# Kernel optimization log

Measured on AMD Instinct MI355X. Metric: run time of the kernel, lower is better.

The kernel has to match this reference:

```python
import jax, jax.numpy as jnp
import numpy as np

EMBED = 64
HEADS = 8
N, S = 8, 1024


def setup_inputs() -> dict:
    key = jax.random.key(0)
    ks = jax.random.split(key, 8)
    scale = 1.0 / np.sqrt(EMBED)
    return {
        "values": jax.random.normal(ks[0], (N, S, EMBED), dtype=jnp.float32),
        "keys": jax.random.normal(ks[1], (N, S, EMBED), dtype=jnp.float32),
        "queries": jax.random.normal(ks[2], (N, S, EMBED), dtype=jnp.float32),
        # per-head projection weights, torch Linear convention: y = x @ W.T
        "Wv": jax.random.normal(ks[3], (HEADS, EMBED, EMBED), dtype=jnp.float32) * scale,
        "Wk": jax.random.normal(ks[4], (HEADS, EMBED, EMBED), dtype=jnp.float32) * scale,
        "Wq": jax.random.normal(ks[5], (HEADS, EMBED, EMBED), dtype=jnp.float32) * scale,
        "Wout": jax.random.normal(ks[6], (EMBED, HEADS * EMBED), dtype=jnp.float32) * (1.0 / np.sqrt(HEADS * EMBED)),
        "bout": jnp.zeros((EMBED,), dtype=jnp.float32),
    }


def reference(values, keys, queries, Wv, Wk, Wq, Wout, bout):
    d = queries.shape[-1]
    # Batched per-head projections (each head keeps full embed dim, per the module)
    v = jnp.einsum("nkd,hed->nhke", values, Wv)   # [N,H,K,D]
    k = jnp.einsum("nkd,hed->nhke", keys, Wk)     # [N,H,K,D]
    q = jnp.einsum("nqd,hed->nhqe", queries, Wq)  # [N,H,Q,D]
    energy = jnp.einsum("nhqd,nhkd->nhqk", q, k)
    attn = jax.nn.softmax(energy / jnp.sqrt(jnp.asarray(d, energy.dtype)), axis=-1)  # [N,H,Q,K]
    head_out = jnp.einsum("nhqk,nhkd->nhqd", attn, v)  # [N,H,Q,D]
    # torch.cat(output_heads, dim=2) == transpose heads next to feature then flatten
    nN, nH, nQ, nD = head_out.shape
    cat = jnp.transpose(head_out, (0, 2, 1, 3)).reshape(nN, nQ, nH * nD)  # [N,Q,H*D]
    out = cat @ Wout.T + bout  # [N,Q,D]
    return out, attn
```

## Files before the change

### kernel.cpp

```cpp
#include <hip/hip_runtime.h>

typedef __bf16 bf16x8 __attribute__((ext_vector_type(8)));
typedef __bf16 bf16x4 __attribute__((ext_vector_type(4)));
typedef float  f32x4  __attribute__((ext_vector_type(4)));

#define MFMA16(a, b, c) __builtin_amdgcn_mfma_f32_16x16x32_bf16((a), (b), (c), 0, 0, 0)

constexpr int N_ = 8, H_ = 8, S_ = 1024, D_ = 64;

__global__ __launch_bounds__(256) void proj_kernel(
    const float* __restrict__ Xq, const float* __restrict__ Xk,
    const float* __restrict__ Xv,
    const float* __restrict__ Wq, const float* __restrict__ Wk,
    const float* __restrict__ Wv,
    unsigned short* __restrict__ qb_, unsigned short* __restrict__ kb_,
    unsigned short* __restrict__ vtb_)
{
    __shared__ __bf16 T[64 * 72];

    const int which = blockIdx.y;
    const float* X = (which == 0) ? Xq : (which == 1) ? Xk : Xv;
    const float* W = (which == 0) ? Wq : (which == 1) ? Wk : Wv;

    const int b   = blockIdx.x;
    const int st  = b & 15;
    const int h   = (b >> 4) & 7;
    const int n   = b >> 7;
    const int s0  = st * 64;
    const int nh  = n * H_ + h;
    const int tid = threadIdx.x;
    const int w = tid >> 6, lane = tid & 63;
    const int l16 = lane & 15, quad = lane >> 4;

    const float* xrow = X + (size_t)(n * S_ + s0 + w * 16 + l16) * D_;
    bf16x8 a[2];
#pragma unroll
    for (int half = 0; half < 2; ++half) {
        const float* p = xrow + half * 32 + quad * 8;
        f32x4 x0 = *(const f32x4*)p;
        f32x4 x1 = *(const f32x4*)(p + 4);
#pragma unroll
        for (int j = 0; j < 4; ++j) { a[half][j] = (__bf16)x0[j]; a[half][4 + j] = (__bf16)x1[j]; }
    }

#pragma unroll
    for (int et = 0; et < 4; ++et) {
        const int e0 = et * 16;
        f32x4 acc = {0.f, 0.f, 0.f, 0.f};
#pragma unroll
        for (int half = 0; half < 2; ++half) {
            const float* wp = W + ((size_t)(h * 64 + e0 + l16)) * 64 + half * 32 + quad * 8;
            f32x4 x0 = *(const f32x4*)wp;
            f32x4 x1 = *(const f32x4*)(wp + 4);
            bf16x8 bf;
#pragma unroll
            for (int j = 0; j < 4; ++j) { bf[j] = (__bf16)x0[j]; bf[4 + j] = (__bf16)x1[j]; }
            acc = MFMA16(a[half], bf, acc);
        }
#pragma unroll
        for (int r = 0; r < 4; ++r) {
            const int sl = w * 16 + quad * 4 + r;
            const int e  = e0 + l16;
            const __bf16 v = (__bf16)acc[r];
            if (which == 2) T[e * 72 + sl] = v;
            else            T[sl * 72 + e] = v;
        }
    }
    __syncthreads();

    const int row = tid >> 2, seg = tid & 3;
    const bf16x8 d0 = *(const bf16x8*)&T[row * 72 + seg * 16];
    const bf16x8 d1 = *(const bf16x8*)&T[row * 72 + seg * 16 + 8];
    __bf16* dst;
    if (which == 2)
        dst = (__bf16*)vtb_ + ((size_t)nh * 64 + row) * S_ + s0 + seg * 16;
    else
        dst = (__bf16*)(which == 0 ? qb_ : kb_) + ((size_t)nh * S_ + s0 + row) * D_ + seg * 16;
    *(bf16x8*)dst = d0;
    *(bf16x8*)(dst + 8) = d1;
}

__global__ __launch_bounds__(256, 8) void attn_kernel(
    const unsigned short* __restrict__ qb_, const unsigned short* __restrict__ kb_,
    const unsigned short* __restrict__ vtb_,
    float* __restrict__ attn_out, unsigned short* __restrict__ catb_)
{
    __shared__ float Sred[4 * 16];
    __shared__ float Ored[2 * 16 * 68];

    const __bf16* qb  = (const __bf16*)qb_;
    const __bf16* kb  = (const __bf16*)kb_;
    const __bf16* vtb = (const __bf16*)vtb_;
    __bf16* catb = (__bf16*)catb_;

    const int bid = blockIdx.x;
    const int b   = (bid & 7) * 256 + (bid >> 3);
    const int qt  = b & 31;
    const int h   = (b >> 5) & 7;
    const int n   = b >> 8;
    const int nh  = n * H_ + h;
    const int q0  = qt * 32;

    const int tid = threadIdx.x;
    const int w = tid >> 6, lane = tid & 63;
    const int l16 = lane & 15, quad = lane >> 4;
    const int rw = w & 1;
    const int kw = w >> 1;
    const int k0 = kw * 512;

    const __bf16* qbase = qb + ((size_t)(nh * S_ + q0 + rw * 16 + l16)) * D_;
    const bf16x8 aq0 = *(const bf16x8*)(qbase + quad * 8);
    const bf16x8 aq1 = *(const bf16x8*)(qbase + 32 + quad * 8);

    const __bf16* kbase = kb + ((size_t)(nh * S_ + k0 + l16)) * D_ + quad * 8;

    float ssum = 0.f;
#pragma unroll 4
    for (int kt = 0; kt < 32; ++kt) {
        const __bf16* kp = kbase + (size_t)kt * 16 * D_;
        const bf16x8 b0 = *(const bf16x8*)kp;
        const bf16x8 b1 = *(const bf16x8*)(kp + 32);
        f32x4 c = {0.f, 0.f, 0.f, 0.f};
        c = MFMA16(b0, aq0, c);
        c = MFMA16(b1, aq1, c);
#pragma unroll
        for (int r = 0; r < 4; ++r) ssum += __expf(c[r] * 0.125f);
    }
    ssum += __shfl_xor(ssum, 16);
    ssum += __shfl_xor(ssum, 32);
    if (lane < 16) Sred[w * 16 + lane] = ssum;
    __syncthreads();
    const float inv = 1.0f / (Sred[w * 16 + l16] + Sred[(w ^ 2) * 16 + l16]);

    float* abase = attn_out + ((size_t)(nh * S_ + q0 + rw * 16 + l16)) * S_ + k0;
    const __bf16* vbase = vtb + ((size_t)(nh * 64 + l16)) * S_ + k0 + quad * 8;

    const int lo_addr = (((quad & 1) * 2) * 16 + l16) * 4;
    const int hi_addr = lo_addr + 64;
    const bool hiq = (quad & 2) != 0;

    f32x4 acc[4] = {{0.f,0.f,0.f,0.f},{0.f,0.f,0.f,0.f},{0.f,0.f,0.f,0.f},{0.f,0.f,0.f,0.f}};

#pragma unroll 2
    for (int ch = 0; ch < 16; ++ch) {
        unsigned Wt[2][2];
#pragma unroll
        for (int t = 0; t < 2; ++t) {
            const int kt = ch * 2 + t;
            const __bf16* kp = kbase + (size_t)kt * 16 * D_;
            const bf16x8 b0 = *(const bf16x8*)kp;
            const bf16x8 b1 = *(const bf16x8*)(kp + 32);
            f32x4 c = {0.f, 0.f, 0.f, 0.f};
            c = MFMA16(b0, aq0, c);
            c = MFMA16(b1, aq1, c);
            float p[4];
#pragma unroll
            for (int r = 0; r < 4; ++r) p[r] = __expf(c[r] * 0.125f) * inv;
#pragma unroll
            for (int pr = 0; pr < 2; ++pr) {
                const __bf16 ha = (__bf16)p[2 * pr], hb = (__bf16)p[2 * pr + 1];
                const unsigned ua = *(const unsigned short*)&ha;
                const unsigned ub = *(const unsigned short*)&hb;
                Wt[t][pr] = ua | (ub << 16);
            }
        }
        const int s00 = __builtin_amdgcn_ds_bpermute(lo_addr, (int)Wt[0][0]);
        const int s10 = __builtin_amdgcn_ds_bpermute(lo_addr, (int)Wt[1][0]);
        const int s01 = __builtin_amdgcn_ds_bpermute(lo_addr, (int)Wt[0][1]);
        const int s11 = __builtin_amdgcn_ds_bpermute(lo_addr, (int)Wt[1][1]);
        const int s02 = __builtin_amdgcn_ds_bpermute(hi_addr, (int)Wt[0][0]);
        const int s12 = __builtin_amdgcn_ds_bpermute(hi_addr, (int)Wt[1][0]);
        const int s03 = __builtin_amdgcn_ds_bpermute(hi_addr, (int)Wt[0][1]);
        const int s13 = __builtin_amdgcn_ds_bpermute(hi_addr, (int)Wt[1][1]);
        union { bf16x8 v; unsigned u[4]; } pf;
        pf.u[0] = (unsigned)(hiq ? s10 : s00);
        pf.u[1] = (unsigned)(hiq ? s11 : s01);
        pf.u[2] = (unsigned)(hiq ? s12 : s02);
        pf.u[3] = (unsigned)(hiq ? s13 : s03);

#pragma unroll
        for (int et = 0; et < 4; ++et) {
            const bf16x8 bv = *(const bf16x8*)(vbase + (size_t)et * 16 * S_ + ch * 32);
            acc[et] = MFMA16(pf.v, bv, acc[et]);
        }

        f32x4 f0, f1;
#pragma unroll
        for (int j = 0; j < 4; ++j) { f0[j] = (float)pf.v[j]; f1[j] = (float)pf.v[4 + j]; }
        float* ap = abase + ch * 32 + quad * 8;
        *(f32x4*)ap = f0;
        *(f32x4*)(ap + 4) = f1;
    }

    __syncthreads();
    if (kw == 1) {
#pragma unroll
        for (int et = 0; et < 4; ++et)
#pragma unroll
            for (int r = 0; r < 4; ++r)
                Ored[rw * (16 * 68) + (quad * 4 + r) * 68 + et * 16 + l16] = acc[et][r];
    }
    __syncthreads();
    if (kw == 0) {
#pragma unroll
        for (int r = 0; r < 4; ++r) {
            const int s = q0 + rw * 16 + quad * 4 + r;
            __bf16* cp = catb + ((size_t)n * S_ + s) * (H_ * D_) + h * D_ + l16;
#pragma unroll
            for (int et = 0; et < 4; ++et) {
                const float o = acc[et][r] +
                    Ored[rw * (16 * 68) + (quad * 4 + r) * 68 + et * 16 + l16];
                cp[et * 16] = (__bf16)o;
            }
        }
    }
}

__global__ __launch_bounds__(256) void outproj_kernel(
    const unsigned short* __restrict__ catb_, const float* __restrict__ Wout,
    const float* __restrict__ bout, float* __restrict__ out)
{
    __shared__ float R[4 * 16 * 68];

    const __bf16* catb = (const __bf16*)catb_;
    const int r0  = blockIdx.x * 16;
    const int tid = threadIdx.x;
    const int w = tid >> 6, lane = tid & 63;
    const int l16 = lane & 15, quad = lane >> 4;
    const int k0 = w * 128;

    const __bf16* arow  = catb + (size_t)(r0 + l16) * 512 + k0 + quad * 8;
    const float*  wbase = Wout + (size_t)l16 * 512 + k0 + quad * 8;

    f32x4 acc[4] = {{0.f,0.f,0.f,0.f},{0.f,0.f,0.f,0.f},{0.f,0.f,0.f,0.f},{0.f,0.f,0.f,0.f}};

#pragma unroll
    for (int kc = 0; kc < 4; ++kc) {
        const bf16x8 af = *(const bf16x8*)(arow + kc * 32);
#pragma unroll
        for (int et = 0; et < 4; ++et) {
            const float* wp = wbase + (size_t)et * 16 * 512 + kc * 32;
            f32x4 x0 = *(const f32x4*)wp;
            f32x4 x1 = *(const f32x4*)(wp + 4);
            bf16x8 bf;
#pragma unroll
            for (int j = 0; j < 4; ++j) { bf[j] = (__bf16)x0[j]; bf[4 + j] = (__bf16)x1[j]; }
            acc[et] = MFMA16(af, bf, acc[et]);
        }
    }
#pragma unroll
    for (int et = 0; et < 4; ++et)
#pragma unroll
        for (int r = 0; r < 4; ++r)
            R[w * (16 * 68) + (quad * 4 + r) * 68 + et * 16 + l16] = acc[et][r];
    __syncthreads();

    const int row = tid >> 4, c0 = (tid & 15) * 4;
    f32x4 s = *(const f32x4*)&R[row * 68 + c0];
#pragma unroll
    for (int wv = 1; wv < 4; ++wv) s += *(const f32x4*)&R[wv * (16 * 68) + row * 68 + c0];
    s += *(const f32x4*)(bout + c0);
    *(f32x4*)(out + (size_t)(r0 + row) * 64 + c0) = s;
}

extern "C" void kernel_launch(void* const* d_in, const int* in_sizes, int n_in,
                              void* d_out, int out_size, void* d_ws, size_t ws_size,
                              hipStream_t stream)
{
    const float* values  = (const float*)d_in[0];
    const float* keys    = (const float*)d_in[1];
    const float* queries = (const float*)d_in[2];
    const float* Wv      = (const float*)d_in[3];
    const float* Wk      = (const float*)d_in[4];
    const float* Wq      = (const float*)d_in[5];
    const float* Wout    = (const float*)d_in[6];
    const float* bout    = (const float*)d_in[7];

    float* out  = (float*)d_out;
    float* attn = out + (size_t)N_ * S_ * D_;

    const size_t nelem = (size_t)N_ * H_ * S_ * D_;
    unsigned short* qb   = (unsigned short*)d_ws;
    unsigned short* kb   = qb  + nelem;
    unsigned short* vtb  = kb  + nelem;
    unsigned short* catb = vtb + nelem;

    proj_kernel<<<dim3(N_ * H_ * (S_ / 64), 3), 256, 0, stream>>>(
        queries, keys, values, Wq, Wk, Wv, qb, kb, vtb);
    attn_kernel<<<N_ * H_ * (S_ / 32), 256, 0, stream>>>(qb, kb, vtb, attn, catb);
    outproj_kernel<<<(N_ * S_) / 16, 256, 0, stream>>>(catb, Wout, bout, out);
}
```

Before: 482.7 us.

## Store K and V projections in MFMA-fragment order for contiguous wave loads

The projection kernel now writes K and V^T in a pre-swizzled layout, so each 16x32 MFMA operand fragment is stored as 64 contiguous 16-byte chunks indexed by lane. The attention kernel then loads K and V fragments with fully coalesced lane*8 addressing instead of strided row reads. This aims to cut memory transactions and cache-line waste on the K/V operand loads, which happen in both the sum pass and the output pass. It couples the two kernels to a custom layout that is harder to maintain.

```diff
diff --git a/kernel.cpp b/kernel.cpp
--- a/kernel.cpp
+++ b/kernel.cpp
@@ -68,16 +68,38 @@
     }
     __syncthreads();
 
-    const int row = tid >> 2, seg = tid & 3;
-    const bf16x8 d0 = *(const bf16x8*)&T[row * 72 + seg * 16];
-    const bf16x8 d1 = *(const bf16x8*)&T[row * 72 + seg * 16 + 8];
-    __bf16* dst;
-    if (which == 2)
-        dst = (__bf16*)vtb_ + ((size_t)nh * 64 + row) * S_ + s0 + seg * 16;
-    else
-        dst = (__bf16*)(which == 0 ? qb_ : kb_) + ((size_t)nh * S_ + s0 + row) * D_ + seg * 16;
-    *(bf16x8*)dst = d0;
-    *(bf16x8*)(dst + 8) = d1;
+    if (which == 0) {
+        const int row = tid >> 2, seg = tid & 3;
+        const bf16x8 d0 = *(const bf16x8*)&T[row * 72 + seg * 16];
+        const bf16x8 d1 = *(const bf16x8*)&T[row * 72 + seg * 16 + 8];
+        __bf16* dst = (__bf16*)qb_ + ((size_t)nh * S_ + s0 + row) * D_ + seg * 16;
+        *(bf16x8*)dst = d0;
+        *(bf16x8*)(dst + 8) = d1;
+    } else if (which == 1) {
+#pragma unroll
+        for (int cc = 0; cc < 2; ++cc) {
+            const int c   = tid + cc * 256;
+            const int ktl = c >> 7;
+            const int h2  = (c >> 6) & 1;
+            const int ll  = c & 63;
+            const bf16x8 d = *(const bf16x8*)&T[(ktl * 16 + (ll & 15)) * 72 + h2 * 32 + (ll >> 4) * 8];
+            __bf16* dst = (__bf16*)kb_ +
+                (((size_t)(nh * 64 + st * 4 + ktl) * 2 + h2) * 512 + ll * 8);
+            *(bf16x8*)dst = d;
+        }
+    } else {
+#pragma unroll
+        for (int cc = 0; cc < 2; ++cc) {
+            const int c   = tid + cc * 256;
+            const int chl = c >> 8;
+            const int et  = (c >> 6) & 3;
+            const int lv  = c & 63;
+            const bf16x8 d = *(const bf16x8*)&T[(et * 16 + (lv & 15)) * 72 + chl * 32 + (lv >> 4) * 8];
+            __bf16* dst = (__bf16*)vtb_ + (size_t)nh * 65536 +
+                ((size_t)(st * 2 + chl) * 2048 + et * 512 + lv * 8);
+            *(bf16x8*)dst = d;
+        }
+    }
 }
 
 __global__ __launch_bounds__(256, 8) void attn_kernel(
@@ -112,14 +134,14 @@
     const bf16x8 aq0 = *(const bf16x8*)(qbase + quad * 8);
     const bf16x8 aq1 = *(const bf16x8*)(qbase + 32 + quad * 8);
 
-    const __bf16* kbase = kb + ((size_t)(nh * S_ + k0 + l16)) * D_ + quad * 8;
+    const __bf16* kfrag = kb + ((size_t)(nh * 64 + kw * 32)) * 1024 + lane * 8;
 
     float ssum = 0.f;
 #pragma unroll 4
     for (int kt = 0; kt < 32; ++kt) {
-        const __bf16* kp = kbase + (size_t)kt * 16 * D_;
+        const __bf16* kp = kfrag + kt * 1024;
         const bf16x8 b0 = *(const bf16x8*)kp;
-        const bf16x8 b1 = *(const bf16x8*)(kp + 32);
+        const bf16x8 b1 = *(const bf16x8*)(kp + 512);
         f32x4 c = {0.f, 0.f, 0.f, 0.f};
         c = MFMA16(b0, aq0, c);
         c = MFMA16(b1, aq1, c);
@@ -133,7 +155,7 @@
     const float inv = 1.0f / (Sred[w * 16 + l16] + Sred[(w ^ 2) * 16 + l16]);
 
     float* abase = attn_out + ((size_t)(nh * S_ + q0 + rw * 16 + l16)) * S_ + k0;
-    const __bf16* vbase = vtb + ((size_t)(nh * 64 + l16)) * S_ + k0 + quad * 8;
+    const __bf16* vfrag = vtb + (size_t)nh * 65536 + (size_t)kw * 16 * 2048 + lane * 8;
 
     const int lo_addr = (((quad & 1) * 2) * 16 + l16) * 4;
     const int hi_addr = lo_addr + 64;
@@ -147,9 +169,9 @@
 #pragma unroll
         for (int t = 0; t < 2; ++t) {
             const int kt = ch * 2 + t;
-            const __bf16* kp = kbase + (size_t)kt * 16 * D_;
+            const __bf16* kp = kfrag + kt * 1024;
             const bf16x8 b0 = *(const bf16x8*)kp;
-            const bf16x8 b1 = *(const bf16x8*)(kp + 32);
+            const bf16x8 b1 = *(const bf16x8*)(kp + 512);
             f32x4 c = {0.f, 0.f, 0.f, 0.f};
             c = MFMA16(b0, aq0, c);
             c = MFMA16(b1, aq1, c);
@@ -180,7 +202,7 @@
 
 #pragma unroll
         for (int et = 0; et < 4; ++et) {
-            const bf16x8 bv = *(const bf16x8*)(vbase + (size_t)et * 16 * S_ + ch * 32);
+            const bf16x8 bv = *(const bf16x8*)(vfrag + ch * 2048 + et * 512);
             acc[et] = MFMA16(pf.v, bv, acc[et]);
         }
 
```

After: 392.9 us. -18.6%, faster.
